# Kernel tuning notes

Hardware: AMD Instinct MI355X
Metric: run time of the kernel (lower is better)

The kernel has to match this reference:

```python
import jax, jax.numpy as jnp
import numpy as np

B, S, H = 2, 2048, 2048
NH, HD = 16, 128


def _rope_tables(seq_len, dim, base=10000.0):
    inv_freq = 1.0 / (base ** (np.arange(0, dim, 2, dtype=np.float32) / dim))
    t = np.arange(seq_len, dtype=np.float32)
    freqs = np.outer(t, inv_freq)                      # [S, dim/2]
    emb = np.concatenate([freqs, freqs], axis=-1)      # [S, dim] (HF convention)
    return jnp.asarray(np.cos(emb)), jnp.asarray(np.sin(emb))


def setup_inputs() -> dict:
    key = jax.random.key(0)
    k1, k2, k3, k4, k5 = jax.random.split(key, 5)
    hidden_states = jax.random.normal(k1, (B, S, H), dtype=jnp.float32)
    # additive causal mask, broadcast over heads: (B, 1, S, S)
    causal = jnp.tril(jnp.ones((S, S), dtype=bool))
    attention_mask = jnp.where(causal, 0.0, -1e9).astype(jnp.float32)
    attention_mask = jnp.broadcast_to(attention_mask[None, None], (B, 1, S, S))
    rope_cos, rope_sin = _rope_tables(S, HD)
    scale = 1.0 / np.sqrt(H)
    Wq = jax.random.normal(k2, (H, H), dtype=jnp.float32) * scale
    Wk = jax.random.normal(k3, (H, H), dtype=jnp.float32) * scale
    Wv = jax.random.normal(k4, (H, H), dtype=jnp.float32) * scale
    Wo = jax.random.normal(k5, (H, H), dtype=jnp.float32) * scale
    return dict(hidden_states=hidden_states, attention_mask=attention_mask,
                rope_cos=rope_cos, rope_sin=rope_sin, Wq=Wq, Wk=Wk, Wv=Wv, Wo=Wo)


def _rotate_half(x):
    half = x.shape[-1] // 2
    return jnp.concatenate([-x[..., half:], x[..., :half]], axis=-1)


def reference(hidden_states, attention_mask, rope_cos, rope_sin, Wq, Wk, Wv, Wo):
    bsz, q_len, _ = hidden_states.shape
    scaling = HD ** -0.5
    # projections (torch Linear: y = x @ W.T)
    q = (hidden_states @ Wq.T).reshape(bsz, q_len, NH, HD).transpose(0, 2, 1, 3)
    k = (hidden_states @ Wk.T).reshape(bsz, q_len, NH, HD).transpose(0, 2, 1, 3)
    v = (hidden_states @ Wv.T).reshape(bsz, q_len, NH, HD).transpose(0, 2, 1, 3)
    # RoPE (rotate_half convention)
    cos = rope_cos[None, None]  # [1,1,S,HD]
    sin = rope_sin[None, None]
    q = q * cos + _rotate_half(q) * sin
    k = k * cos + _rotate_half(k) * sin
    # attention
    scores = jnp.einsum('bhqd,bhkd->bhqk', q, k) * scaling + attention_mask
    attn = jax.nn.softmax(scores.astype(jnp.float32), axis=-1).astype(q.dtype)
    out = jnp.einsum('bhqk,bhkd->bhqd', attn, v)
    out = out.transpose(0, 2, 1, 3).reshape(bsz, q_len, NH * HD)
    return out @ Wo.T
```

## Files before the change

### kernel.cpp

```cpp
#include <hip/hip_runtime.h>
#include <hip/hip_bf16.h>

typedef __bf16 bf16;
typedef __attribute__((ext_vector_type(8))) __bf16 bf16x8;
typedef __attribute__((ext_vector_type(4))) __bf16 bf16x4;
typedef __attribute__((ext_vector_type(4))) float f32x4;

#define BB 2
#define SS 2048
#define HH 2048
#define NH 16
#define HD 128

#define GLOAD_LDS16(g, l)                                                  \
    __builtin_amdgcn_global_load_lds(                                      \
        (const __attribute__((address_space(1))) void*)(g),                \
        (__attribute__((address_space(3))) void*)(l), 16, 0, 0)

__global__ __launch_bounds__(256) void cast_all(const float* __restrict__ hs,
                                                const float* __restrict__ Wq,
                                                const float* __restrict__ Wk,
                                                const float* __restrict__ Wv,
                                                const float* __restrict__ Wo,
                                                bf16* __restrict__ Xb,
                                                bf16* __restrict__ Wqkv,
                                                bf16* __restrict__ Wob) {
    const int XE4 = (BB * SS * HH) / 4;
    const int WE4 = (HH * HH) / 4;
    int i = blockIdx.x * 256 + threadIdx.x;
    const float* src;
    bf16* dst;
    int off;
    if (i < XE4) { src = hs; dst = Xb; off = i; }
    else if (i < XE4 + WE4) { src = Wq; dst = Wqkv; off = i - XE4; }
    else if (i < XE4 + 2 * WE4) { src = Wk; dst = Wqkv + (size_t)HH * HH; off = i - XE4 - WE4; }
    else if (i < XE4 + 3 * WE4) { src = Wv; dst = Wqkv + 2 * (size_t)HH * HH; off = i - XE4 - 2 * WE4; }
    else { src = Wo; dst = Wob; off = i - XE4 - 3 * WE4; }
    f32x4 v = *reinterpret_cast<const f32x4*>(src + (size_t)off * 4);
    bf16x4 o;
    o[0] = (bf16)v[0]; o[1] = (bf16)v[1]; o[2] = (bf16)v[2]; o[3] = (bf16)v[3];
    *reinterpret_cast<bf16x4*>(dst + (size_t)off * 4) = o;
}

__global__ __launch_bounds__(512, 2) void gemm256_qkv(const bf16* __restrict__ A,
                                                      const bf16* __restrict__ B,
                                                      bf16* __restrict__ Cb,
                                                      int M, int N, int K) {
    __shared__ bf16 LA[2][256 * 64];
    __shared__ bf16 LB[2][256 * 64];
    const int tid = threadIdx.x, lane = tid & 63, wave = tid >> 6;
    const int l15 = lane & 15, lhi = lane >> 4;
    const int wr = wave >> 2, wc = wave & 3;
    const int NBX = N >> 8;
    const int cpx = gridDim.x >> 3;
    const int wg = (blockIdx.x & 7) * cpx + (blockIdx.x >> 3);
    const int m0 = (wg / NBX) * 256, n0 = (wg % NBX) * 256;
    const int NK = K >> 6;
    const int xorR = (l15 & 7) << 4;

    auto stageA = [&](int buf, int t, int h) {
        const int k0 = t << 6;
#pragma unroll
        for (int j = 0; j < 2; ++j) {
            int Xw = ((j * 128 + h * 64) << 7) + (wave << 10);
            int X = Xw + lane * 16;
            int T = X ^ (((X >> 7) & 7) << 4);
            GLOAD_LDS16(&A[(size_t)(m0 + (T >> 7)) * K + k0 + ((T & 127) >> 1)],
                        (char*)LA[buf] + Xw);
        }
    };
    auto stageB = [&](int buf, int t, int h) {
        const int k0 = t << 6;
#pragma unroll
        for (int j = 0; j < 2; ++j) {
            int base_row = h * 32 + (2 * j + (wave >> 2)) * 64;
            int Xw = (base_row << 7) + ((wave & 3) << 10);
            int X = Xw + lane * 16;
            int T = X ^ (((X >> 7) & 7) << 4);
            GLOAD_LDS16(&B[(size_t)(n0 + (T >> 7)) * K + k0 + ((T & 127) >> 1)],
                        (char*)LB[buf] + Xw);
        }
    };

    f32x4 acc[8][4] = {};

    stageA(0, 0, 0); stageB(0, 0, 0); stageB(0, 0, 1); stageA(0, 0, 1);
    stageA(1, 1, 0); stageB(1, 1, 1);
    asm volatile("s_waitcnt vmcnt(4)" ::: "memory");
    __builtin_amdgcn_s_barrier();

    bf16x8 af[4][2], bv0[2][2], bv1[2][2];

#pragma unroll 1
    for (int t = 0; t < NK; ++t) {
        const int buf = t & 1;
        char* lA = (char*)LA[buf];
        char* lB = (char*)LB[buf];

#pragma unroll
        for (int f = 0; f < 4; ++f)
#pragma unroll
            for (int ks = 0; ks < 2; ++ks) {
                int T = ((wr * 128 + f * 16 + l15) << 7) + ks * 64 + lhi * 16;
                af[f][ks] = *reinterpret_cast<const bf16x8*>(lA + (T ^ xorR));
            }
#pragma unroll
        for (int g = 0; g < 2; ++g)
#pragma unroll
            for (int ks = 0; ks < 2; ++ks) {
                int T = ((wc * 64 + g * 16 + l15) << 7) + ks * 64 + lhi * 16;
                bv0[g][ks] = *reinterpret_cast<const bf16x8*>(lB + (T ^ xorR));
            }
        if (t + 1 < NK) stageB(buf ^ 1, t + 1, 0);
        __builtin_amdgcn_s_barrier();
        asm volatile("s_waitcnt lgkmcnt(0)" ::: "memory");
        __builtin_amdgcn_s_setprio(1);
#pragma unroll
        for (int f = 0; f < 4; ++f)
#pragma unroll
            for (int g = 0; g < 2; ++g)
#pragma unroll
                for (int ks = 0; ks < 2; ++ks)
                    acc[f][g] = __builtin_amdgcn_mfma_f32_16x16x32_bf16(af[f][ks], bv0[g][ks], acc[f][g], 0, 0, 0);
        __builtin_amdgcn_s_setprio(0);
        __builtin_amdgcn_s_barrier();

#pragma unroll
        for (int g = 0; g < 2; ++g)
#pragma unroll
            for (int ks = 0; ks < 2; ++ks) {
                int T = ((wc * 64 + 32 + g * 16 + l15) << 7) + ks * 64 + lhi * 16;
                bv1[g][ks] = *reinterpret_cast<const bf16x8*>(lB + (T ^ xorR));
            }
        if (t + 1 < NK) stageA(buf ^ 1, t + 1, 1);
        __builtin_amdgcn_s_barrier();
        asm volatile("s_waitcnt lgkmcnt(0)" ::: "memory");
        __builtin_amdgcn_s_setprio(1);
#pragma unroll
        for (int f = 0; f < 4; ++f)
#pragma unroll
            for (int g = 0; g < 2; ++g)
#pragma unroll
                for (int ks = 0; ks < 2; ++ks)
                    acc[f][2 + g] = __builtin_amdgcn_mfma_f32_16x16x32_bf16(af[f][ks], bv1[g][ks], acc[f][2 + g], 0, 0, 0);
        __builtin_amdgcn_s_setprio(0);
        __builtin_amdgcn_s_barrier();

#pragma unroll
        for (int f = 0; f < 4; ++f)
#pragma unroll
            for (int ks = 0; ks < 2; ++ks) {
                int T = ((wr * 128 + 64 + f * 16 + l15) << 7) + ks * 64 + lhi * 16;
                af[f][ks] = *reinterpret_cast<const bf16x8*>(lA + (T ^ xorR));
            }
        if (t + 2 < NK) stageA(buf, t + 2, 0);
        __builtin_amdgcn_s_barrier();
        asm volatile("s_waitcnt lgkmcnt(0)" ::: "memory");
        __builtin_amdgcn_s_setprio(1);
#pragma unroll
        for (int f = 0; f < 4; ++f)
#pragma unroll
            for (int g = 0; g < 2; ++g)
#pragma unroll
                for (int ks = 0; ks < 2; ++ks)
                    acc[4 + f][2 + g] = __builtin_amdgcn_mfma_f32_16x16x32_bf16(af[f][ks], bv1[g][ks], acc[4 + f][2 + g], 0, 0, 0);
        __builtin_amdgcn_s_setprio(0);
        __builtin_amdgcn_s_barrier();

        if (t + 2 < NK) stageB(buf, t + 2, 1);
        __builtin_amdgcn_s_barrier();
        __builtin_amdgcn_s_setprio(1);
#pragma unroll
        for (int f = 0; f < 4; ++f)
#pragma unroll
            for (int g = 0; g < 2; ++g)
#pragma unroll
                for (int ks = 0; ks < 2; ++ks)
                    acc[4 + f][g] = __builtin_amdgcn_mfma_f32_16x16x32_bf16(af[f][ks], bv0[g][ks], acc[4 + f][g], 0, 0, 0);
        __builtin_amdgcn_s_setprio(0);
        if (t + 2 == NK) {
            asm volatile("s_waitcnt vmcnt(0)" ::: "memory");
        } else if (t + 1 < NK) {
            asm volatile("s_waitcnt vmcnt(4)" ::: "memory");
        }
        __builtin_amdgcn_s_barrier();
    }

#pragma unroll
    for (int mf = 0; mf < 8; ++mf)
#pragma unroll
        for (int nf = 0; nf < 4; ++nf)
#pragma unroll
            for (int r = 0; r < 4; ++r) {
                int gm = m0 + wr * 128 + mf * 16 + lhi * 4 + r;
                int gn = n0 + wc * 64 + nf * 16 + l15;
                int proj = gn >> 11, n2 = gn & 2047;
                int b = gm >> 11, s = gm & (SS - 1);
                int h = n2 >> 7, d = n2 & (HD - 1);
                Cb[((size_t)proj << 23) + ((((size_t)(b * NH + h)) * SS + s) << 7) + d] =
                    (bf16)acc[mf][nf][r];
            }
}

__global__ __launch_bounds__(256) void gemm_bt(const bf16* __restrict__ A,
                                               const bf16* __restrict__ B,
                                               float* __restrict__ Cf,
                                               int M, int N, int K) {
    __shared__ bf16 As[128 * 64];
    __shared__ bf16 Bs[128 * 64];
    const int tid = threadIdx.x;
    const int lane = tid & 63, wave = tid >> 6;
    const int l15 = lane & 15, lhi = lane >> 4;
    const int m0 = blockIdx.y * 128, n0 = blockIdx.x * 128;
    const int wm = (wave >> 1) * 64, wn = (wave & 1) * 64;
    const int lrow = lane >> 3;
    const int lcol = (lane & 7) * 8;

    f32x4 acc[4][4] = {};

    for (int k0 = 0; k0 < K; k0 += 64) {
#pragma unroll
        for (int j = 0; j < 4; ++j) {
            const int c = wave * 4 + j;
            const int row = c * 8 + lrow;
            GLOAD_LDS16(&A[(size_t)(m0 + row) * K + k0 + lcol], &As[c * 512]);
            GLOAD_LDS16(&B[(size_t)(n0 + row) * K + k0 + lcol], &Bs[c * 512]);
        }
        __syncthreads();
#pragma unroll
        for (int ks = 0; ks < 2; ++ks) {
            bf16x8 af[4], bfr[4];
#pragma unroll
            for (int i = 0; i < 4; ++i)
                af[i] = *reinterpret_cast<const bf16x8*>(&As[(wm + i * 16 + l15) * 64 + ks * 32 + 8 * lhi]);
#pragma unroll
            for (int j = 0; j < 4; ++j)
                bfr[j] = *reinterpret_cast<const bf16x8*>(&Bs[(wn + j * 16 + l15) * 64 + ks * 32 + 8 * lhi]);
#pragma unroll
            for (int i = 0; i < 4; ++i)
#pragma unroll
                for (int j = 0; j < 4; ++j)
                    acc[i][j] = __builtin_amdgcn_mfma_f32_16x16x32_bf16(af[i], bfr[j], acc[i][j], 0, 0, 0);
        }
        __syncthreads();
    }

#pragma unroll
    for (int i = 0; i < 4; ++i)
#pragma unroll
        for (int j = 0; j < 4; ++j)
#pragma unroll
            for (int r = 0; r < 4; ++r) {
                int gm = m0 + wm + i * 16 + lhi * 4 + r;
                int gn = n0 + wn + j * 16 + l15;
                Cf[(size_t)gm * N + gn] = acc[i][j][r];
            }
}

__global__ __launch_bounds__(256) void transpose_v(const bf16* __restrict__ Vh,
                                                   bf16* __restrict__ Vt) {
    __shared__ bf16 T[64 * 64];
    const int tid = threadIdx.x;
    const int s0 = blockIdx.x * 64, d0 = blockIdx.y * 64, head = blockIdx.z;
    const bf16* src = Vh + ((size_t)head * SS) * HD;
    bf16* dst = Vt + ((size_t)head * HD) * SS;

#pragma unroll
    for (int i = 0; i < 2; ++i) {
        int id = tid + i * 256;
        int r = id >> 3, c16 = id & 7;
        bf16x8 v = *reinterpret_cast<const bf16x8*>(&src[(size_t)(s0 + r) * HD + d0 + c16 * 8]);
        int sw = c16 ^ ((r ^ (r >> 3)) & 7);
        *reinterpret_cast<bf16x8*>((char*)T + r * 128 + sw * 16) = v;
    }
    __syncthreads();
#pragma unroll
    for (int i = 0; i < 2; ++i) {
        int id = tid + i * 256;
        int dr = id >> 3, sc8 = (id & 7) * 8;
        bf16x8 o;
#pragma unroll
        for (int j = 0; j < 8; ++j) {
            int r = sc8 + j;
            int sw = (dr >> 3) ^ ((r ^ (r >> 3)) & 7);
            o[j] = *reinterpret_cast<const bf16*>((char*)T + r * 128 + sw * 16 + (dr & 7) * 2);
        }
        *reinterpret_cast<bf16x8*>(&dst[(size_t)(d0 + dr) * SS + s0 + sc8]) = o;
    }
}

__global__ __launch_bounds__(256) void rope_kernel(bf16* __restrict__ Qh, bf16* __restrict__ Kh,
                                                   const float* __restrict__ cosT,
                                                   const float* __restrict__ sinT) {
    int idx = blockIdx.x * 256 + threadIdx.x;
    int g = idx & 7;
    int s = (idx >> 3) & (SS - 1);
    int head = idx >> 14;
    int d0 = g * 8;
    size_t base = ((size_t)head * SS + s) * HD;
    f32x4 ca = *reinterpret_cast<const f32x4*>(&cosT[s * HD + d0]);
    f32x4 cb = *reinterpret_cast<const f32x4*>(&cosT[s * HD + d0 + 4]);
    f32x4 sa = *reinterpret_cast<const f32x4*>(&sinT[s * HD + d0]);
    f32x4 sb = *reinterpret_cast<const f32x4*>(&sinT[s * HD + d0 + 4]);
    bf16x8 ql = *reinterpret_cast<const bf16x8*>(&Qh[base + d0]);
    bf16x8 qh = *reinterpret_cast<const bf16x8*>(&Qh[base + 64 + d0]);
    bf16x8 kl = *reinterpret_cast<const bf16x8*>(&Kh[base + d0]);
    bf16x8 kh = *reinterpret_cast<const bf16x8*>(&Kh[base + 64 + d0]);
    bf16x8 qlo, qhi, klo, khi;
#pragma unroll
    for (int j = 0; j < 8; ++j) {
        float c = (j < 4) ? ca[j] : cb[j - 4];
        float sn = (j < 4) ? sa[j] : sb[j - 4];
        float q0 = (float)ql[j], q1 = (float)qh[j];
        float k0 = (float)kl[j], k1 = (float)kh[j];
        qlo[j] = (bf16)(q0 * c - q1 * sn);
        qhi[j] = (bf16)(q1 * c + q0 * sn);
        klo[j] = (bf16)(k0 * c - k1 * sn);
        khi[j] = (bf16)(k1 * c + k0 * sn);
    }
    *reinterpret_cast<bf16x8*>(&Qh[base + d0]) = qlo;
    *reinterpret_cast<bf16x8*>(&Qh[base + 64 + d0]) = qhi;
    *reinterpret_cast<bf16x8*>(&Kh[base + d0]) = klo;
    *reinterpret_cast<bf16x8*>(&Kh[base + 64 + d0]) = khi;
}

__global__ __launch_bounds__(256) void attn_kernel(const bf16* __restrict__ Q,
                                                   const bf16* __restrict__ K,
                                                   const bf16* __restrict__ Vt,
                                                   bf16* __restrict__ Ob) {
    __shared__ bf16 Ks[2][64 * 128];
    __shared__ bf16 Vs[2][128 * 64];
    __shared__ bf16 Ps[4][16][72];

    const int tid = threadIdx.x, lane = tid & 63, wave = tid >> 6;
    const int l15 = lane & 15, lhi = lane >> 4;
    const int bid = blockIdx.x;
    const int orig = (bid & 7) * 64 + (bid >> 3);
    const int head = orig >> 4;
    const int pi = orig & 15;
    const int b = head >> 4, h = head & (NH - 1);
    const size_t hb = (size_t)head * SS * HD;
    const bf16* Vth = Vt + (size_t)head * HD * SS;
    const float cexp = 0.08838834764831845f * 1.4426950408889634f;
    const float THR = 62.0f;

#pragma unroll 1
    for (int part = 0; part < 2; ++part) {
        const int t = part ? (31 - pi) : pi;
        const int q0 = t * 64;
        const int qw = q0 + wave * 16;
        const int nkv = t + 1;

        bf16x8 qf[4];
#pragma unroll
        for (int ks = 0; ks < 4; ++ks)
            qf[ks] = *reinterpret_cast<const bf16x8*>(
                &Q[hb + (size_t)(qw + l15) * HD + ks * 32 + 8 * lhi]);

        f32x4 oacc[8] = {};
        float Mr[4], Lp[4];
#pragma unroll
        for (int r = 0; r < 4; ++r) { Mr[r] = -INFINITY; Lp[r] = 0.f; }

        bf16x8 kr[4], vr[4];
#pragma unroll
        for (int i = 0; i < 4; ++i) {
            int id = tid + i * 256;
            kr[i] = *reinterpret_cast<const bf16x8*>(&K[hb + (size_t)(id >> 4) * HD + (id & 15) * 8]);
            vr[i] = *reinterpret_cast<const bf16x8*>(&Vth[(size_t)(id >> 3) * SS + (id & 7) * 8]);
        }
#pragma unroll
        for (int i = 0; i < 4; ++i) {
            int id = tid + i * 256;
            int krow = id >> 4, kc = id & 15;
            *reinterpret_cast<bf16x8*>((char*)Ks[0] + ((krow * 256 + kc * 16) ^ ((krow & 7) << 4))) = kr[i];
            int vrow = id >> 3, vc = id & 7;
            *reinterpret_cast<bf16x8*>((char*)Vs[0] + ((vrow * 128 + vc * 16) ^ ((vrow & 7) << 4))) = vr[i];
        }
        __syncthreads();

        for (int it = 0; it < nkv; ++it) {
            const int cur = it & 1;
            const bool pre = (it + 1 < nkv);
            if (pre) {
                const int kv0 = (it + 1) * 64;
#pragma unroll
                for (int i = 0; i < 4; ++i) {
                    int id = tid + i * 256;
                    kr[i] = *reinterpret_cast<const bf16x8*>(&K[hb + (size_t)(kv0 + (id >> 4)) * HD + (id & 15) * 8]);
                    vr[i] = *reinterpret_cast<const bf16x8*>(&Vth[(size_t)(id >> 3) * SS + kv0 + (id & 7) * 8]);
                }
            }

            f32x4 sf[4] = {};
#pragma unroll
            for (int ks = 0; ks < 4; ++ks) {
#pragma unroll
                for (int ne = 0; ne < 4; ++ne) {
                    int row = ne * 16 + l15;
                    bf16x8 kf = *reinterpret_cast<const bf16x8*>(
                        (const char*)Ks[cur] + ((row * 256 + (ks * 4 + lhi) * 16) ^ ((row & 7) << 4)));
                    sf[ne] = __builtin_amdgcn_mfma_f32_16x16x32_bf16(qf[ks], kf, sf[ne], 0, 0, 0);
                }
            }

            if (it == nkv - 1) {
#pragma unroll
                for (int ne = 0; ne < 4; ++ne)
#pragma unroll
                    for (int r = 0; r < 4; ++r) {
                        int gq = qw + lhi * 4 + r;
                        int gk = it * 64 + ne * 16 + l15;
                        if (gk > gq) sf[ne][r] = -INFINITY;
                    }
            }

            float lm[4];
#pragma unroll
            for (int r = 0; r < 4; ++r)
                lm[r] = fmaxf(fmaxf(sf[0][r], sf[1][r]), fmaxf(sf[2][r], sf[3][r]));
            bool need = (lm[0] > Mr[0] + THR) || (lm[1] > Mr[1] + THR) ||
                        (lm[2] > Mr[2] + THR) || (lm[3] > Mr[3] + THR);
            if (__any(need)) {
                float rmax[4] = {lm[0], lm[1], lm[2], lm[3]};
#pragma unroll
                for (int m = 1; m < 16; m <<= 1)
#pragma unroll
                    for (int r = 0; r < 4; ++r)
                        rmax[r] = fmaxf(rmax[r], __shfl_xor(rmax[r], m));
#pragma unroll
                for (int r = 0; r < 4; ++r) {
                    float nM = fmaxf(Mr[r], rmax[r]);
                    float scf = __builtin_amdgcn_exp2f((Mr[r] - nM) * cexp);
                    Mr[r] = nM;
                    Lp[r] *= scf;
#pragma unroll
                    for (int nf = 0; nf < 8; ++nf) oacc[nf][r] *= scf;
                }
            }
#pragma unroll
            for (int ne = 0; ne < 4; ++ne)
#pragma unroll
                for (int r = 0; r < 4; ++r) {
                    float p = __builtin_amdgcn_exp2f((sf[ne][r] - Mr[r]) * cexp);
                    Lp[r] += p;
                    Ps[wave][lhi * 4 + r][ne * 16 + l15] = (bf16)p;
                }

#pragma unroll
            for (int ks = 0; ks < 2; ++ks) {
                bf16x8 pa = *reinterpret_cast<const bf16x8*>(&Ps[wave][l15][ks * 32 + 8 * lhi]);
#pragma unroll
                for (int nf = 0; nf < 8; ++nf) {
                    int row = nf * 16 + l15;
                    bf16x8 vb = *reinterpret_cast<const bf16x8*>(
                        (const char*)Vs[cur] + ((row * 128 + (ks * 4 + lhi) * 16) ^ ((row & 7) << 4)));
                    oacc[nf] = __builtin_amdgcn_mfma_f32_16x16x32_bf16(pa, vb, oacc[nf], 0, 0, 0);
                }
            }

            if (pre) {
#pragma unroll
                for (int i = 0; i < 4; ++i) {
                    int id = tid + i * 256;
                    int krow = id >> 4, kc = id & 15;
                    *reinterpret_cast<bf16x8*>((char*)Ks[cur ^ 1] + ((krow * 256 + kc * 16) ^ ((krow & 7) << 4))) = kr[i];
                    int vrow = id >> 3, vc = id & 7;
                    *reinterpret_cast<bf16x8*>((char*)Vs[cur ^ 1] + ((vrow * 128 + vc * 16) ^ ((vrow & 7) << 4))) = vr[i];
                }
            }
            __syncthreads();
        }

#pragma unroll
        for (int m = 1; m < 16; m <<= 1)
#pragma unroll
            for (int r = 0; r < 4; ++r)
                Lp[r] += __shfl_xor(Lp[r], m);
        float inv[4];
#pragma unroll
        for (int r = 0; r < 4; ++r) inv[r] = 1.f / Lp[r];
#pragma unroll
        for (int nf = 0; nf < 8; ++nf)
#pragma unroll
            for (int r = 0; r < 4; ++r) {
                int s = qw + lhi * 4 + r;
                int d = nf * 16 + l15;
                Ob[((size_t)(b * SS + s)) * HH + h * HD + d] = (bf16)(oacc[nf][r] * inv[r]);
            }
    }
}

extern "C" void kernel_launch(void* const* d_in, const int* in_sizes, int n_in,
                              void* d_out, int out_size, void* d_ws, size_t ws_size,
                              hipStream_t stream) {
    const float* hs   = (const float*)d_in[0];
    const float* cosT = (const float*)d_in[2];
    const float* sinT = (const float*)d_in[3];
    const float* Wq   = (const float*)d_in[4];
    const float* Wk   = (const float*)d_in[5];
    const float* Wv   = (const float*)d_in[6];
    const float* Wo   = (const float*)d_in[7];
    float* out = (float*)d_out;

    char* w = (char*)d_ws;
    auto alloc = [&](size_t bytes) {
        char* p = w;
        w += (bytes + 255) & ~(size_t)255;
        return p;
    };
    const size_t XE = (size_t)BB * SS * HH;
    const size_t WE = (size_t)HH * HH;
    bf16* Xb   = (bf16*)alloc(XE * 2);
    bf16* Wqkv = (bf16*)alloc(3 * WE * 2);
    bf16* Wob  = (bf16*)alloc(WE * 2);
    bf16* QKV  = (bf16*)alloc(3 * XE * 2);
    bf16* Vtg  = (bf16*)alloc(XE * 2);
    bf16* Ob   = (bf16*)alloc(XE * 2);

    const int M = BB * SS;
    bf16* Qh = QKV;
    bf16* Kh = QKV + XE;
    bf16* Vh = QKV + 2 * XE;

    {
        int total4 = (int)((XE + 4 * WE) / 4);
        cast_all<<<(total4 + 255) / 256, 256, 0, stream>>>(hs, Wq, Wk, Wv, Wo, Xb, Wqkv, Wob);
    }

    gemm256_qkv<<<dim3((M / 256) * (3 * HH / 256)), 512, 0, stream>>>(Xb, Wqkv, QKV, M, 3 * HH, HH);

    rope_kernel<<<(BB * NH * SS * 8) / 256, 256, 0, stream>>>(Qh, Kh, cosT, sinT);

    dim3 tgrid(SS / 64, HD / 64, BB * NH);
    transpose_v<<<tgrid, 256, 0, stream>>>(Vh, Vtg);

    attn_kernel<<<512, 256, 0, stream>>>(Qh, Kh, Vtg, Ob);

    dim3 ogrid(HH / 128, M / 128);
    gemm_bt<<<ogrid, 256, 0, stream>>>(Ob, Wob, out, M, HH, HH);
}
```

Before: 301.7 us.

## Shrink QKV GEMM tile to 128x256 and reuse it for output projection

Replaces the 256x256 QKV GEMM with a templated 128x256 tile kernel, which doubles the number of workgroups and halves A-tile LDS and accumulator registers. The same pipelined kernel, with an fp32 epilogue, now also runs the output projection instead of the simple 128x128 gemm_bt without double buffering. The prefetch schedule is reworked to load the B halves and the A tile two iterations ahead, with vmcnt adjusted to 6. The risk is lower arithmetic intensity per tile in the QKV GEMM in exchange for better CU occupancy and load balance.

```diff
diff --git a/kernel.cpp b/kernel.cpp
--- a/kernel.cpp
+++ b/kernel.cpp
@@ -42,11 +42,13 @@
     *reinterpret_cast<bf16x4*>(dst + (size_t)off * 4) = o;
 }
 
-__global__ __launch_bounds__(512, 2) void gemm256_qkv(const bf16* __restrict__ A,
+template <int EPI>
+__global__ __launch_bounds__(512, 2) void gemm128x256(const bf16* __restrict__ A,
                                                       const bf16* __restrict__ B,
+                                                      float* __restrict__ Cf,
                                                       bf16* __restrict__ Cb,
                                                       int M, int N, int K) {
-    __shared__ bf16 LA[2][256 * 64];
+    __shared__ bf16 LA[2][128 * 64];
     __shared__ bf16 LB[2][256 * 64];
     const int tid = threadIdx.x, lane = tid & 63, wave = tid >> 6;
     const int l15 = lane & 15, lhi = lane >> 4;
@@ -54,15 +56,15 @@
     const int NBX = N >> 8;
     const int cpx = gridDim.x >> 3;
     const int wg = (blockIdx.x & 7) * cpx + (blockIdx.x >> 3);
-    const int m0 = (wg / NBX) * 256, n0 = (wg % NBX) * 256;
+    const int m0 = (wg / NBX) * 128, n0 = (wg % NBX) * 256;
     const int NK = K >> 6;
     const int xorR = (l15 & 7) << 4;
 
-    auto stageA = [&](int buf, int t, int h) {
+    auto stageA = [&](int buf, int t) {
         const int k0 = t << 6;
 #pragma unroll
         for (int j = 0; j < 2; ++j) {
-            int Xw = ((j * 128 + h * 64) << 7) + (wave << 10);
+            int Xw = j * 8192 + wave * 1024;
             int X = Xw + lane * 16;
             int T = X ^ (((X >> 7) & 7) << 4);
             GLOAD_LDS16(&A[(size_t)(m0 + (T >> 7)) * K + k0 + ((T & 127) >> 1)],
@@ -82,26 +84,27 @@
         }
     };
 
-    f32x4 acc[8][4] = {};
-
-    stageA(0, 0, 0); stageB(0, 0, 0); stageB(0, 0, 1); stageA(0, 0, 1);
-    stageA(1, 1, 0); stageB(1, 1, 1);
-    asm volatile("s_waitcnt vmcnt(4)" ::: "memory");
+    f32x4 acc[4][4] = {};
+
+    stageB(0, 0, 0); stageB(0, 0, 1); stageA(0, 0);
+    stageB(1, 1, 0); stageB(1, 1, 1); stageA(1, 1);
+    asm volatile("s_waitcnt vmcnt(6)" ::: "memory");
     __builtin_amdgcn_s_barrier();
 
-    bf16x8 af[4][2], bv0[2][2], bv1[2][2];
+    bf16x8 af[2][2], bv0[2][2], bv1[2][2];
 
 #pragma unroll 1
     for (int t = 0; t < NK; ++t) {
         const int buf = t & 1;
         char* lA = (char*)LA[buf];
         char* lB = (char*)LB[buf];
-
-#pragma unroll
-        for (int f = 0; f < 4; ++f)
+        const bool pre = (t + 2 < NK);
+
+#pragma unroll
+        for (int f = 0; f < 2; ++f)
 #pragma unroll
             for (int ks = 0; ks < 2; ++ks) {
-                int T = ((wr * 128 + f * 16 + l15) << 7) + ks * 64 + lhi * 16;
+                int T = ((wr * 64 + f * 16 + l15) << 7) + ks * 64 + lhi * 16;
                 af[f][ks] = *reinterpret_cast<const bf16x8*>(lA + (T ^ xorR));
             }
 #pragma unroll
@@ -111,12 +114,11 @@
                 int T = ((wc * 64 + g * 16 + l15) << 7) + ks * 64 + lhi * 16;
                 bv0[g][ks] = *reinterpret_cast<const bf16x8*>(lB + (T ^ xorR));
             }
-        if (t + 1 < NK) stageB(buf ^ 1, t + 1, 0);
         __builtin_amdgcn_s_barrier();
         asm volatile("s_waitcnt lgkmcnt(0)" ::: "memory");
         __builtin_amdgcn_s_setprio(1);
 #pragma unroll
-        for (int f = 0; f < 4; ++f)
+        for (int f = 0; f < 2; ++f)
 #pragma unroll
             for (int g = 0; g < 2; ++g)
 #pragma unroll
@@ -132,12 +134,12 @@
                 int T = ((wc * 64 + 32 + g * 16 + l15) << 7) + ks * 64 + lhi * 16;
                 bv1[g][ks] = *reinterpret_cast<const bf16x8*>(lB + (T ^ xorR));
             }
-        if (t + 1 < NK) stageA(buf ^ 1, t + 1, 1);
+        if (pre) stageB(buf, t + 2, 0);
         __builtin_amdgcn_s_barrier();
         asm volatile("s_waitcnt lgkmcnt(0)" ::: "memory");
         __builtin_amdgcn_s_setprio(1);
 #pragma unroll
-        for (int f = 0; f < 4; ++f)
+        for (int f = 0; f < 2; ++f)
 #pragma unroll
             for (int g = 0; g < 2; ++g)
 #pragma unroll
@@ -147,113 +149,62 @@
         __builtin_amdgcn_s_barrier();
 
 #pragma unroll
-        for (int f = 0; f < 4; ++f)
+        for (int f = 0; f < 2; ++f)
 #pragma unroll
             for (int ks = 0; ks < 2; ++ks) {
-                int T = ((wr * 128 + 64 + f * 16 + l15) << 7) + ks * 64 + lhi * 16;
+                int T = ((wr * 64 + 32 + f * 16 + l15) << 7) + ks * 64 + lhi * 16;
                 af[f][ks] = *reinterpret_cast<const bf16x8*>(lA + (T ^ xorR));
             }
-        if (t + 2 < NK) stageA(buf, t + 2, 0);
+        if (pre) stageB(buf, t + 2, 1);
         __builtin_amdgcn_s_barrier();
         asm volatile("s_waitcnt lgkmcnt(0)" ::: "memory");
         __builtin_amdgcn_s_setprio(1);
 #pragma unroll
-        for (int f = 0; f < 4; ++f)
+        for (int f = 0; f < 2; ++f)
 #pragma unroll
             for (int g = 0; g < 2; ++g)
 #pragma unroll
                 for (int ks = 0; ks < 2; ++ks)
-                    acc[4 + f][2 + g] = __builtin_amdgcn_mfma_f32_16x16x32_bf16(af[f][ks], bv1[g][ks], acc[4 + f][2 + g], 0, 0, 0);
+                    acc[2 + f][2 + g] = __builtin_amdgcn_mfma_f32_16x16x32_bf16(af[f][ks], bv1[g][ks], acc[2 + f][2 + g], 0, 0, 0);
         __builtin_amdgcn_s_setprio(0);
         __builtin_amdgcn_s_barrier();
 
-        if (t + 2 < NK) stageB(buf, t + 2, 1);
+        if (pre) stageA(buf, t + 2);
         __builtin_amdgcn_s_barrier();
         __builtin_amdgcn_s_setprio(1);
 #pragma unroll
-        for (int f = 0; f < 4; ++f)
+        for (int f = 0; f < 2; ++f)
 #pragma unroll
             for (int g = 0; g < 2; ++g)
 #pragma unroll
                 for (int ks = 0; ks < 2; ++ks)
-                    acc[4 + f][g] = __builtin_amdgcn_mfma_f32_16x16x32_bf16(af[f][ks], bv0[g][ks], acc[4 + f][g], 0, 0, 0);
+                    acc[2 + f][g] = __builtin_amdgcn_mfma_f32_16x16x32_bf16(af[f][ks], bv0[g][ks], acc[2 + f][g], 0, 0, 0);
         __builtin_amdgcn_s_setprio(0);
         if (t + 2 == NK) {
             asm volatile("s_waitcnt vmcnt(0)" ::: "memory");
-        } else if (t + 1 < NK) {
-            asm volatile("s_waitcnt vmcnt(4)" ::: "memory");
-        }
-        __builtin_amdgcn_s_barrier();
-    }
-
-#pragma unroll
-    for (int mf = 0; mf < 8; ++mf)
+        } else if (t + 2 < NK) {
+            asm volatile("s_waitcnt vmcnt(6)" ::: "memory");
+        }
+        __builtin_amdgcn_s_barrier();
+    }
+
+#pragma unroll
+    for (int mf = 0; mf < 4; ++mf)
 #pragma unroll
         for (int nf = 0; nf < 4; ++nf)
 #pragma unroll
             for (int r = 0; r < 4; ++r) {
-                int gm = m0 + wr * 128 + mf * 16 + lhi * 4 + r;
+                int gm = m0 + wr * 64 + mf * 16 + lhi * 4 + r;
                 int gn = n0 + wc * 64 + nf * 16 + l15;
-                int proj = gn >> 11, n2 = gn & 2047;
-                int b = gm >> 11, s = gm & (SS - 1);
-                int h = n2 >> 7, d = n2 & (HD - 1);
-                Cb[((size_t)proj << 23) + ((((size_t)(b * NH + h)) * SS + s) << 7) + d] =
-                    (bf16)acc[mf][nf][r];
-            }
-}
-
-__global__ __launch_bounds__(256) void gemm_bt(const bf16* __restrict__ A,
-                                               const bf16* __restrict__ B,
-                                               float* __restrict__ Cf,
-                                               int M, int N, int K) {
-    __shared__ bf16 As[128 * 64];
-    __shared__ bf16 Bs[128 * 64];
-    const int tid = threadIdx.x;
-    const int lane = tid & 63, wave = tid >> 6;
-    const int l15 = lane & 15, lhi = lane >> 4;
-    const int m0 = blockIdx.y * 128, n0 = blockIdx.x * 128;
-    const int wm = (wave >> 1) * 64, wn = (wave & 1) * 64;
-    const int lrow = lane >> 3;
-    const int lcol = (lane & 7) * 8;
-
-    f32x4 acc[4][4] = {};
-
-    for (int k0 = 0; k0 < K; k0 += 64) {
-#pragma unroll
-        for (int j = 0; j < 4; ++j) {
-            const int c = wave * 4 + j;
-            const int row = c * 8 + lrow;
-            GLOAD_LDS16(&A[(size_t)(m0 + row) * K + k0 + lcol], &As[c * 512]);
-            GLOAD_LDS16(&B[(size_t)(n0 + row) * K + k0 + lcol], &Bs[c * 512]);
-        }
-        __syncthreads();
-#pragma unroll
-        for (int ks = 0; ks < 2; ++ks) {
-            bf16x8 af[4], bfr[4];
-#pragma unroll
-            for (int i = 0; i < 4; ++i)
-                af[i] = *reinterpret_cast<const bf16x8*>(&As[(wm + i * 16 + l15) * 64 + ks * 32 + 8 * lhi]);
-#pragma unroll
-            for (int j = 0; j < 4; ++j)
-                bfr[j] = *reinterpret_cast<const bf16x8*>(&Bs[(wn + j * 16 + l15) * 64 + ks * 32 + 8 * lhi]);
-#pragma unroll
-            for (int i = 0; i < 4; ++i)
-#pragma unroll
-                for (int j = 0; j < 4; ++j)
-                    acc[i][j] = __builtin_amdgcn_mfma_f32_16x16x32_bf16(af[i], bfr[j], acc[i][j], 0, 0, 0);
-        }
-        __syncthreads();
-    }
-
-#pragma unroll
-    for (int i = 0; i < 4; ++i)
-#pragma unroll
-        for (int j = 0; j < 4; ++j)
-#pragma unroll
-            for (int r = 0; r < 4; ++r) {
-                int gm = m0 + wm + i * 16 + lhi * 4 + r;
-                int gn = n0 + wn + j * 16 + l15;
-                Cf[(size_t)gm * N + gn] = acc[i][j][r];
+                if (EPI == 0) {
+                    int proj = gn >> 11, n2 = gn & 2047;
+                    int b = gm >> 11, s = gm & (SS - 1);
+                    int h = n2 >> 7, d = n2 & (HD - 1);
+                    Cb[((size_t)proj << 23) + ((((size_t)(b * NH + h)) * SS + s) << 7) + d] =
+                        (bf16)acc[mf][nf][r];
+                } else {
+                    Cf[(size_t)gm * N + gn] = acc[mf][nf][r];
+                }
             }
 }
 
@@ -528,7 +479,8 @@
         cast_all<<<(total4 + 255) / 256, 256, 0, stream>>>(hs, Wq, Wk, Wv, Wo, Xb, Wqkv, Wob);
     }
 
-    gemm256_qkv<<<dim3((M / 256) * (3 * HH / 256)), 512, 0, stream>>>(Xb, Wqkv, QKV, M, 3 * HH, HH);
+    gemm128x256<0><<<dim3((M / 128) * (3 * HH / 256)), 512, 0, stream>>>(
+        Xb, Wqkv, nullptr, QKV, M, 3 * HH, HH);
 
     rope_kernel<<<(BB * NH * SS * 8) / 256, 256, 0, stream>>>(Qh, Kh, cosT, sinT);
 
@@ -537,6 +489,6 @@
 
     attn_kernel<<<512, 256, 0, stream>>>(Qh, Kh, Vtg, Ob);
 
-    dim3 ogrid(HH / 128, M / 128);
-    gemm_bt<<<ogrid, 256, 0, stream>>>(Ob, Wob, out, M, HH, HH);
-}
+    gemm128x256<1><<<dim3((M / 128) * (HH / 256)), 512, 0, stream>>>(
+        Ob, Wob, out, nullptr, M, HH, HH);
+}
```

New measurement: 324.9 us. 1.08x slower.

## Restructure attention to 128-row query tiles with 8 waves and staggered K/V prefetch

Applied to the files above, without the earlier changes.

The attention kernel now uses 512-thread blocks covering 128 query rows per block, with one tile per block instead of two 64-row tiles processed in sequence. Each K/V tile loaded from global memory is therefore shared by twice as many query rows. V is single-buffered and written to LDS after the QK softmax phase, with an extra barrier per iteration. K is prefetched two tiles ahead and V one tile ahead, cutting the per-thread prefetch registers. The goal is less K/V traffic per query and better latency hiding, at the cost of more barriers and coarser causal load balancing.

```diff
diff --git a/kernel.cpp b/kernel.cpp
--- a/kernel.cpp
+++ b/kernel.cpp
@@ -324,171 +324,168 @@
     *reinterpret_cast<bf16x8*>(&Kh[base + 64 + d0]) = khi;
 }
 
-__global__ __launch_bounds__(256) void attn_kernel(const bf16* __restrict__ Q,
-                                                   const bf16* __restrict__ K,
-                                                   const bf16* __restrict__ Vt,
-                                                   bf16* __restrict__ Ob) {
+__global__ __launch_bounds__(512, 4) void attn_kernel(const bf16* __restrict__ Q,
+                                                      const bf16* __restrict__ K,
+                                                      const bf16* __restrict__ Vt,
+                                                      bf16* __restrict__ Ob) {
     __shared__ bf16 Ks[2][64 * 128];
-    __shared__ bf16 Vs[2][128 * 64];
-    __shared__ bf16 Ps[4][16][72];
+    __shared__ bf16 Vs[128 * 64];
+    __shared__ bf16 Ps[8][16 * 72];
 
     const int tid = threadIdx.x, lane = tid & 63, wave = tid >> 6;
     const int l15 = lane & 15, lhi = lane >> 4;
-    const int bid = blockIdx.x;
-    const int orig = (bid & 7) * 64 + (bid >> 3);
-    const int head = orig >> 4;
-    const int pi = orig & 15;
+    const int p = blockIdx.x & 255;
+    const int head = p >> 3;
+    const int Tl = p & 7;
+    const int T = (blockIdx.x >> 8) ? (15 - Tl) : Tl;
     const int b = head >> 4, h = head & (NH - 1);
     const size_t hb = (size_t)head * SS * HD;
     const bf16* Vth = Vt + (size_t)head * HD * SS;
     const float cexp = 0.08838834764831845f * 1.4426950408889634f;
     const float THR = 62.0f;
 
+    const int q0 = T * 128;
+    const int qw = q0 + wave * 16;
+    const int nkv = 2 * T + 2;
+
+    const int ka0 = tid >> 4, kc0 = (tid & 15) * 8;
+    const int ka1 = (tid + 512) >> 4, kc1 = ((tid + 512) & 15) * 8;
+    const int va0 = tid >> 3, vc0 = (tid & 7) * 8;
+    const int va1 = (tid + 512) >> 3, vc1 = ((tid + 512) & 7) * 8;
+    const int ksw0 = (ka0 * 256 + kc0 * 2) ^ ((ka0 & 7) << 4);
+    const int ksw1 = (ka1 * 256 + kc1 * 2) ^ ((ka1 & 7) << 4);
+    const int vsw0 = (va0 * 128 + vc0 * 2) ^ ((va0 & 7) << 4);
+    const int vsw1 = (va1 * 128 + vc1 * 2) ^ ((va1 & 7) << 4);
+
+    bf16x8 qf[4];
+#pragma unroll
+    for (int ks = 0; ks < 4; ++ks)
+        qf[ks] = *reinterpret_cast<const bf16x8*>(
+            &Q[hb + (size_t)(qw + l15) * HD + ks * 32 + 8 * lhi]);
+
+    f32x4 oacc[8] = {};
+    float Mr[4], Lp[4];
+#pragma unroll
+    for (int r = 0; r < 4; ++r) { Mr[r] = -INFINITY; Lp[r] = 0.f; }
+
+    bf16x8 kr0 = *reinterpret_cast<const bf16x8*>(&K[hb + (size_t)ka0 * HD + kc0]);
+    bf16x8 kr1 = *reinterpret_cast<const bf16x8*>(&K[hb + (size_t)ka1 * HD + kc1]);
+    bf16x8 vr0 = *reinterpret_cast<const bf16x8*>(&Vth[(size_t)va0 * SS + vc0]);
+    bf16x8 vr1 = *reinterpret_cast<const bf16x8*>(&Vth[(size_t)va1 * SS + vc1]);
+    *reinterpret_cast<bf16x8*>((char*)Ks[0] + ksw0) = kr0;
+    *reinterpret_cast<bf16x8*>((char*)Ks[0] + ksw1) = kr1;
+    kr0 = *reinterpret_cast<const bf16x8*>(&K[hb + (size_t)(64 + ka0) * HD + kc0]);
+    kr1 = *reinterpret_cast<const bf16x8*>(&K[hb + (size_t)(64 + ka1) * HD + kc1]);
+    __syncthreads();
+
 #pragma unroll 1
-    for (int part = 0; part < 2; ++part) {
-        const int t = part ? (31 - pi) : pi;
-        const int q0 = t * 64;
-        const int qw = q0 + wave * 16;
-        const int nkv = t + 1;
-
-        bf16x8 qf[4];
-#pragma unroll
-        for (int ks = 0; ks < 4; ++ks)
-            qf[ks] = *reinterpret_cast<const bf16x8*>(
-                &Q[hb + (size_t)(qw + l15) * HD + ks * 32 + 8 * lhi]);
-
-        f32x4 oacc[8] = {};
-        float Mr[4], Lp[4];
-#pragma unroll
-        for (int r = 0; r < 4; ++r) { Mr[r] = -INFINITY; Lp[r] = 0.f; }
-
-        bf16x8 kr[4], vr[4];
-#pragma unroll
-        for (int i = 0; i < 4; ++i) {
-            int id = tid + i * 256;
-            kr[i] = *reinterpret_cast<const bf16x8*>(&K[hb + (size_t)(id >> 4) * HD + (id & 15) * 8]);
-            vr[i] = *reinterpret_cast<const bf16x8*>(&Vth[(size_t)(id >> 3) * SS + (id & 7) * 8]);
-        }
-#pragma unroll
-        for (int i = 0; i < 4; ++i) {
-            int id = tid + i * 256;
-            int krow = id >> 4, kc = id & 15;
-            *reinterpret_cast<bf16x8*>((char*)Ks[0] + ((krow * 256 + kc * 16) ^ ((krow & 7) << 4))) = kr[i];
-            int vrow = id >> 3, vc = id & 7;
-            *reinterpret_cast<bf16x8*>((char*)Vs[0] + ((vrow * 128 + vc * 16) ^ ((vrow & 7) << 4))) = vr[i];
-        }
+    for (int it = 0; it < nkv; ++it) {
+        const int cur = it & 1;
+
+        f32x4 sf[4] = {};
+#pragma unroll
+        for (int ks = 0; ks < 4; ++ks) {
+#pragma unroll
+            for (int ne = 0; ne < 4; ++ne) {
+                int row = ne * 16 + l15;
+                bf16x8 kf = *reinterpret_cast<const bf16x8*>(
+                    (const char*)Ks[cur] + ((row * 256 + (ks * 4 + lhi) * 16) ^ ((row & 7) << 4)));
+                sf[ne] = __builtin_amdgcn_mfma_f32_16x16x32_bf16(qf[ks], kf, sf[ne], 0, 0, 0);
+            }
+        }
+
+        if (it + 2 >= nkv) {
+#pragma unroll
+            for (int ne = 0; ne < 4; ++ne)
+#pragma unroll
+                for (int r = 0; r < 4; ++r) {
+                    int gq = qw + lhi * 4 + r;
+                    int gk = it * 64 + ne * 16 + l15;
+                    if (gk > gq) sf[ne][r] = -INFINITY;
+                }
+        }
+
+        float lm[4];
+#pragma unroll
+        for (int r = 0; r < 4; ++r)
+            lm[r] = fmaxf(fmaxf(sf[0][r], sf[1][r]), fmaxf(sf[2][r], sf[3][r]));
+        bool need = (lm[0] > Mr[0] + THR) || (lm[1] > Mr[1] + THR) ||
+                    (lm[2] > Mr[2] + THR) || (lm[3] > Mr[3] + THR);
+        if (__any(need)) {
+            float rmax[4] = {lm[0], lm[1], lm[2], lm[3]};
+#pragma unroll
+            for (int m = 1; m < 16; m <<= 1)
+#pragma unroll
+                for (int r = 0; r < 4; ++r)
+                    rmax[r] = fmaxf(rmax[r], __shfl_xor(rmax[r], m));
+#pragma unroll
+            for (int r = 0; r < 4; ++r) {
+                float nM = fmaxf(Mr[r], rmax[r]);
+                float scf = __builtin_amdgcn_exp2f((Mr[r] - nM) * cexp);
+                Mr[r] = nM;
+                Lp[r] *= scf;
+#pragma unroll
+                for (int nf = 0; nf < 8; ++nf) oacc[nf][r] *= scf;
+            }
+        }
+#pragma unroll
+        for (int ne = 0; ne < 4; ++ne)
+#pragma unroll
+            for (int r = 0; r < 4; ++r) {
+                float pv = __builtin_amdgcn_exp2f((sf[ne][r] - Mr[r]) * cexp);
+                Lp[r] += pv;
+                Ps[wave][(lhi * 4 + r) * 72 + ne * 16 + l15] = (bf16)pv;
+            }
+
         __syncthreads();
 
-        for (int it = 0; it < nkv; ++it) {
-            const int cur = it & 1;
-            const bool pre = (it + 1 < nkv);
-            if (pre) {
-                const int kv0 = (it + 1) * 64;
-#pragma unroll
-                for (int i = 0; i < 4; ++i) {
-                    int id = tid + i * 256;
-                    kr[i] = *reinterpret_cast<const bf16x8*>(&K[hb + (size_t)(kv0 + (id >> 4)) * HD + (id & 15) * 8]);
-                    vr[i] = *reinterpret_cast<const bf16x8*>(&Vth[(size_t)(id >> 3) * SS + kv0 + (id & 7) * 8]);
-                }
-            }
-
-            f32x4 sf[4] = {};
-#pragma unroll
-            for (int ks = 0; ks < 4; ++ks) {
-#pragma unroll
-                for (int ne = 0; ne < 4; ++ne) {
-                    int row = ne * 16 + l15;
-                    bf16x8 kf = *reinterpret_cast<const bf16x8*>(
-                        (const char*)Ks[cur] + ((row * 256 + (ks * 4 + lhi) * 16) ^ ((row & 7) << 4)));
-                    sf[ne] = __builtin_amdgcn_mfma_f32_16x16x32_bf16(qf[ks], kf, sf[ne], 0, 0, 0);
-                }
-            }
-
-            if (it == nkv - 1) {
-#pragma unroll
-                for (int ne = 0; ne < 4; ++ne)
-#pragma unroll
-                    for (int r = 0; r < 4; ++r) {
-                        int gq = qw + lhi * 4 + r;
-                        int gk = it * 64 + ne * 16 + l15;
-                        if (gk > gq) sf[ne][r] = -INFINITY;
-                    }
-            }
-
-            float lm[4];
-#pragma unroll
-            for (int r = 0; r < 4; ++r)
-                lm[r] = fmaxf(fmaxf(sf[0][r], sf[1][r]), fmaxf(sf[2][r], sf[3][r]));
-            bool need = (lm[0] > Mr[0] + THR) || (lm[1] > Mr[1] + THR) ||
-                        (lm[2] > Mr[2] + THR) || (lm[3] > Mr[3] + THR);
-            if (__any(need)) {
-                float rmax[4] = {lm[0], lm[1], lm[2], lm[3]};
-#pragma unroll
-                for (int m = 1; m < 16; m <<= 1)
-#pragma unroll
-                    for (int r = 0; r < 4; ++r)
-                        rmax[r] = fmaxf(rmax[r], __shfl_xor(rmax[r], m));
-#pragma unroll
-                for (int r = 0; r < 4; ++r) {
-                    float nM = fmaxf(Mr[r], rmax[r]);
-                    float scf = __builtin_amdgcn_exp2f((Mr[r] - nM) * cexp);
-                    Mr[r] = nM;
-                    Lp[r] *= scf;
-#pragma unroll
-                    for (int nf = 0; nf < 8; ++nf) oacc[nf][r] *= scf;
-                }
-            }
-#pragma unroll
-            for (int ne = 0; ne < 4; ++ne)
-#pragma unroll
-                for (int r = 0; r < 4; ++r) {
-                    float p = __builtin_amdgcn_exp2f((sf[ne][r] - Mr[r]) * cexp);
-                    Lp[r] += p;
-                    Ps[wave][lhi * 4 + r][ne * 16 + l15] = (bf16)p;
-                }
-
-#pragma unroll
-            for (int ks = 0; ks < 2; ++ks) {
-                bf16x8 pa = *reinterpret_cast<const bf16x8*>(&Ps[wave][l15][ks * 32 + 8 * lhi]);
-#pragma unroll
-                for (int nf = 0; nf < 8; ++nf) {
-                    int row = nf * 16 + l15;
-                    bf16x8 vb = *reinterpret_cast<const bf16x8*>(
-                        (const char*)Vs[cur] + ((row * 128 + (ks * 4 + lhi) * 16) ^ ((row & 7) << 4)));
-                    oacc[nf] = __builtin_amdgcn_mfma_f32_16x16x32_bf16(pa, vb, oacc[nf], 0, 0, 0);
-                }
-            }
-
-            if (pre) {
-#pragma unroll
-                for (int i = 0; i < 4; ++i) {
-                    int id = tid + i * 256;
-                    int krow = id >> 4, kc = id & 15;
-                    *reinterpret_cast<bf16x8*>((char*)Ks[cur ^ 1] + ((krow * 256 + kc * 16) ^ ((krow & 7) << 4))) = kr[i];
-                    int vrow = id >> 3, vc = id & 7;
-                    *reinterpret_cast<bf16x8*>((char*)Vs[cur ^ 1] + ((vrow * 128 + vc * 16) ^ ((vrow & 7) << 4))) = vr[i];
-                }
-            }
-            __syncthreads();
-        }
-
-#pragma unroll
-        for (int m = 1; m < 16; m <<= 1)
-#pragma unroll
-            for (int r = 0; r < 4; ++r)
-                Lp[r] += __shfl_xor(Lp[r], m);
-        float inv[4];
-#pragma unroll
-        for (int r = 0; r < 4; ++r) inv[r] = 1.f / Lp[r];
-#pragma unroll
-        for (int nf = 0; nf < 8; ++nf)
-#pragma unroll
-            for (int r = 0; r < 4; ++r) {
-                int s = qw + lhi * 4 + r;
-                int d = nf * 16 + l15;
-                Ob[((size_t)(b * SS + s)) * HH + h * HD + d] = (bf16)(oacc[nf][r] * inv[r]);
-            }
-    }
+        *reinterpret_cast<bf16x8*>((char*)Vs + vsw0) = vr0;
+        *reinterpret_cast<bf16x8*>((char*)Vs + vsw1) = vr1;
+        if (it + 1 < nkv) {
+            *reinterpret_cast<bf16x8*>((char*)Ks[cur ^ 1] + ksw0) = kr0;
+            *reinterpret_cast<bf16x8*>((char*)Ks[cur ^ 1] + ksw1) = kr1;
+            const int kv1 = (it + 1) * 64;
+            vr0 = *reinterpret_cast<const bf16x8*>(&Vth[(size_t)va0 * SS + kv1 + vc0]);
+            vr1 = *reinterpret_cast<const bf16x8*>(&Vth[(size_t)va1 * SS + kv1 + vc1]);
+        }
+        if (it + 2 < nkv) {
+            const int kv2 = (it + 2) * 64;
+            kr0 = *reinterpret_cast<const bf16x8*>(&K[hb + (size_t)(kv2 + ka0) * HD + kc0]);
+            kr1 = *reinterpret_cast<const bf16x8*>(&K[hb + (size_t)(kv2 + ka1) * HD + kc1]);
+        }
+
+        __syncthreads();
+
+#pragma unroll
+        for (int ks = 0; ks < 2; ++ks) {
+            bf16x8 pa = *reinterpret_cast<const bf16x8*>(
+                &Ps[wave][l15 * 72 + ks * 32 + 8 * lhi]);
+#pragma unroll
+            for (int nf = 0; nf < 8; ++nf) {
+                int row = nf * 16 + l15;
+                bf16x8 vb = *reinterpret_cast<const bf16x8*>(
+                    (const char*)Vs + ((row * 128 + (ks * 4 + lhi) * 16) ^ ((row & 7) << 4)));
+                oacc[nf] = __builtin_amdgcn_mfma_f32_16x16x32_bf16(pa, vb, oacc[nf], 0, 0, 0);
+            }
+        }
+    }
+
+#pragma unroll
+    for (int m = 1; m < 16; m <<= 1)
+#pragma unroll
+        for (int r = 0; r < 4; ++r)
+            Lp[r] += __shfl_xor(Lp[r], m);
+    float inv[4];
+#pragma unroll
+    for (int r = 0; r < 4; ++r) inv[r] = 1.f / Lp[r];
+#pragma unroll
+    for (int nf = 0; nf < 8; ++nf)
+#pragma unroll
+        for (int r = 0; r < 4; ++r) {
+            int s = qw + lhi * 4 + r;
+            int d = nf * 16 + l15;
+            Ob[((size_t)(b * SS + s)) * HH + h * HD + d] = (bf16)(oacc[nf][r] * inv[r]);
+        }
 }
 
 extern "C" void kernel_launch(void* const* d_in, const int* in_sizes, int n_in,
@@ -535,7 +532,7 @@
     dim3 tgrid(SS / 64, HD / 64, BB * NH);
     transpose_v<<<tgrid, 256, 0, stream>>>(Vh, Vtg);
 
-    attn_kernel<<<512, 256, 0, stream>>>(Qh, Kh, Vtg, Ob);
+    attn_kernel<<<512, 512, 0, stream>>>(Qh, Kh, Vtg, Ob);
 
     dim3 ogrid(HH / 128, M / 128);
     gemm_bt<<<ogrid, 256, 0, stream>>>(Ob, Wob, out, M, HH, HH);
```

After: 347.4 us. 15.1% more time.
